# Kernel tuning notes

Hardware: AMD Instinct MI355X
Metric: run time of the kernel (lower is better)

The kernel has to match this reference:

```python
import jax, jax.numpy as jnp
import numpy as np

B, N, T_OBS, T_S, D, D_H, P = 32, 256, 50, 25, 128, 256, 8
TWO_PI = 2.0 * np.pi
EPS = 1e-4


def setup_inputs() -> dict:
    key = jax.random.key(0)
    ks = jax.random.split(key, 12)
    s = 0.02
    return {
        "x_ego_mean": jax.random.normal(ks[0], (B, T_OBS, 2), jnp.float32),
        "x_nei_mean": jax.random.normal(ks[1], (B, N, T_OBS, 2), jnp.float32),
        "f_ego": jax.random.normal(ks[2], (B, T_S, D), jnp.float32),
        "f_nei": jax.random.normal(ks[3], (B, N, T_S, D), jnp.float32),
        "W1": s * jax.random.normal(ks[4], (D, D_H), jnp.float32),
        "b1": jnp.zeros((D_H,), jnp.float32),
        "W2": s * jax.random.normal(ks[5], (D_H, D_H), jnp.float32),
        "b2": jnp.zeros((D_H,), jnp.float32),
        "W3": s * jax.random.normal(ks[6], (D_H, D // 2), jnp.float32),
        "b3": jnp.zeros((D // 2,), jnp.float32),
        "Wce": s * jax.random.normal(ks[7], (2, D // 2), jnp.float32),
        "bce": jnp.zeros((D // 2,), jnp.float32),
    }


def reference(x_ego_mean, x_nei_mean, f_ego, f_nei, W1, b1, W2, b2, W3, b3, Wce, bce):
    # --- spectral-similarity feature branch ---
    fn = f_ego[..., None, :, :] * f_nei            # [B, N, T_s, D]
    fn = jnp.max(fn, axis=-3)                      # max over neighbors -> [B, T_s, D]
    h = jax.nn.relu(fn @ W1 + b1)
    h = jax.nn.relu(h @ W2 + b2)
    fn = jax.nn.relu(h @ W3 + b3)                  # [B, T_s, D//2]

    # --- angle-based partitioning of relative positions ---
    t_r = int(np.ceil(x_ego_mean.shape[-2] / f_ego.shape[-2]))  # static stride
    p_nei = x_nei_mean - x_ego_mean[..., None, :, :]            # [B, N, T_obs, 2]
    p_nei = p_nei[..., ::t_r, :]                                # [B, N, T_s, 2]
    f_distance = jnp.linalg.norm(p_nei, axis=-1)                # [B, N, T_s]
    f_angle = jnp.mod(jnp.arctan2(p_nei[..., 0], p_nei[..., 1]), TWO_PI)
    pidx = (f_angle / (TWO_PI / P)).astype(jnp.int32)           # [B, N, T_s]

    nei_mask = (jnp.sum(jnp.abs(p_nei), axis=-1) != 0).astype(jnp.int32)
    non_self_mask = (f_distance > 0.005).astype(jnp.int32)
    final_mask = nei_mask * non_self_mask
    pidx = pidx * final_mask + (-1) * (1 - final_mask)          # invalid -> -1

    # one-hot over partitions replaces the per-partition python loop
    onehot = (pidx[..., None] == jnp.arange(P, dtype=jnp.int32)).astype(f_distance.dtype)  # [B,N,T_s,P]
    counts = jnp.sum(onehot, axis=-3)                           # [B, T_s, P]
    n = counts + EPS
    dist_mean = jnp.sum(f_distance[..., None] * onehot, axis=-3) / n   # [B, T_s, P]
    ang_mean = jnp.sum(f_angle[..., None] * onehot, axis=-3) / n       # [B, T_s, P]

    # original: y_p = sum_N(fn * mask)/n; fn has no N dim, so this is fn * counts / n
    y = fn[..., :, None, :] * (counts / n)[..., None]           # [B, T_s, P, D//2]

    positions = jnp.stack([dist_mean, ang_mean], axis=-1)       # [B, T_s, P, 2]
    pos_enc = jax.nn.relu(positions @ Wce + bce)                # [B, T_s, P, D//2]
    return jnp.concatenate([y, pos_enc], axis=-1)               # [B, T_s, P, D]
```

## Files before the change

### kernel.cpp

```cpp
#include <hip/hip_runtime.h>
#include <math.h>
#include <float.h>

#define B_ 32
#define N_ 256
#define T_OBS_ 50
#define T_S_ 25
#define D_ 128
#define D_H_ 256
#define P_ 8
#define PLANE_ (T_S_ * D_)
#define TG_ 13

static constexpr float TWO_PI_F = 6.2831854820251465f;
static constexpr float BIN_W_F = 0.78539818525314331f;
static constexpr float EPS_F = 1e-4f;

__global__ __launch_bounds__(512) void fused(
    const float* __restrict__ f_ego, const float* __restrict__ f_nei,
    const float* __restrict__ W1, const float* __restrict__ b1,
    const float* __restrict__ W2, const float* __restrict__ b2,
    const float* __restrict__ W3, const float* __restrict__ b3,
    const float* __restrict__ x_ego, const float* __restrict__ x_nei,
    const float* __restrict__ Wce, const float* __restrict__ bce,
    float* __restrict__ out) {
  __shared__ float spool[4096];
  __shared__ float sin_[2][D_];
  __shared__ float sh1[2][D_H_];
  __shared__ float sh2[2][D_H_];
  __shared__ float f3s[2][64];
  __shared__ float whc[8][P_], whd[8][P_], wha[8][P_];
  __shared__ float cnt[2][P_], dsum[2][P_], asum[2][P_];

  const int tid = threadIdx.x;
  const int b = blockIdx.x / TG_;
  const int g = blockIdx.x - b * TG_;
  const int t0 = 2 * g;
  const int t1 = (2 * g + 1 < T_S_) ? (2 * g + 1) : (T_S_ - 1);

  if (tid < 8 * P_) {
    (&whc[0][0])[tid] = 0.f;
    (&whd[0][0])[tid] = 0.f;
    (&wha[0][0])[tid] = 0.f;
  }

  {
    const int sub = tid & 63;
    const int lt = sub >> 5;
    const int d4 = sub & 31;
    const int ng = tid >> 6;
    const int t = lt ? t1 : t0;
    const float4 e =
        *(const float4*)(f_ego + ((size_t)b * T_S_ + t) * D_ + 4 * d4);
    const float* base = f_nei + (size_t)b * N_ * PLANE_ + t * D_ + 4 * d4;
    float4 m = make_float4(-FLT_MAX, -FLT_MAX, -FLT_MAX, -FLT_MAX);
#pragma unroll 16
    for (int i = 0; i < 32; ++i) {
      int n = ng + 8 * i;
      float4 v = *(const float4*)(base + (size_t)n * PLANE_);
      m.x = fmaxf(m.x, e.x * v.x);
      m.y = fmaxf(m.y, e.y * v.y);
      m.z = fmaxf(m.z, e.z * v.z);
      m.w = fmaxf(m.w, e.w * v.w);
    }
    ((float4*)spool)[ng * 64 + sub] = m;
  }

  float2 eg, xn;
  {
    int r = tid >> 8, n = tid & 255;
    int t = r ? t1 : t0;
    int tobs = 2 * t;
    eg = *(const float2*)&x_ego[((size_t)b * T_OBS_ + tobs) * 2];
    xn = *(const float2*)&x_nei[(((size_t)b * N_ + n) * T_OBS_ + tobs) * 2];
  }
  const float bb1 = b1[tid & 255];
  const float bb2 = b2[tid & 255];

  __syncthreads();

  if (tid < 64) {
    float4 r = ((float4*)spool)[tid];
#pragma unroll
    for (int ngg = 1; ngg < 8; ++ngg) {
      float4 v = ((float4*)spool)[ngg * 64 + tid];
      r.x = fmaxf(r.x, v.x);
      r.y = fmaxf(r.y, v.y);
      r.z = fmaxf(r.z, v.z);
      r.w = fmaxf(r.w, v.w);
    }
    *(float4*)&sin_[tid >> 5][4 * (tid & 31)] = r;
  }
  __syncthreads();

  {
    const int s = tid >> 6, j4 = tid & 63;
    const float4* W1v = (const float4*)W1;
    float a[2][4] = {};
#pragma unroll
    for (int kk = 0; kk < 16; ++kk) {
      int k = s * 16 + kk;
      float4 w = W1v[k * 64 + j4];
#pragma unroll
      for (int r = 0; r < 2; ++r) {
        float x = sin_[r][k];
        a[r][0] = fmaf(x, w.x, a[r][0]);
        a[r][1] = fmaf(x, w.y, a[r][1]);
        a[r][2] = fmaf(x, w.z, a[r][2]);
        a[r][3] = fmaf(x, w.w, a[r][3]);
      }
    }
#pragma unroll
    for (int r = 0; r < 2; ++r)
      *(float4*)&spool[(s * 2 + r) * 256 + 4 * j4] =
          make_float4(a[r][0], a[r][1], a[r][2], a[r][3]);
  }
  __syncthreads();
  {
    int r = tid >> 8, j = tid & 255;
    float sum = bb1;
#pragma unroll
    for (int s = 0; s < 8; ++s) sum += spool[(s * 2 + r) * 256 + j];
    sh1[r][j] = fmaxf(sum, 0.f);
  }
  __syncthreads();

  {
    const int s = tid >> 6, j4 = tid & 63;
    const float4* W2v = (const float4*)W2;
    float a[2][4] = {};
#pragma unroll
    for (int kk = 0; kk < 32; ++kk) {
      int k = s * 32 + kk;
      float4 w = W2v[k * 64 + j4];
#pragma unroll
      for (int r = 0; r < 2; ++r) {
        float x = sh1[r][k];
        a[r][0] = fmaf(x, w.x, a[r][0]);
        a[r][1] = fmaf(x, w.y, a[r][1]);
        a[r][2] = fmaf(x, w.z, a[r][2]);
        a[r][3] = fmaf(x, w.w, a[r][3]);
      }
    }
#pragma unroll
    for (int r = 0; r < 2; ++r)
      *(float4*)&spool[(s * 2 + r) * 256 + 4 * j4] =
          make_float4(a[r][0], a[r][1], a[r][2], a[r][3]);
  }
  __syncthreads();
  {
    int r = tid >> 8, j = tid & 255;
    float sum = bb2;
#pragma unroll
    for (int s = 0; s < 8; ++s) sum += spool[(s * 2 + r) * 256 + j];
    sh2[r][j] = fmaxf(sum, 0.f);
  }
  __syncthreads();

  {
    const int s3 = tid >> 4, j4 = tid & 15;
    const float4* W3v = (const float4*)W3;
    float a[2][4] = {};
#pragma unroll
    for (int kk = 0; kk < 8; ++kk) {
      int k = s3 * 8 + kk;
      float4 w = W3v[k * 16 + j4];
#pragma unroll
      for (int r = 0; r < 2; ++r) {
        float x = sh2[r][k];
        a[r][0] = fmaf(x, w.x, a[r][0]);
        a[r][1] = fmaf(x, w.y, a[r][1]);
        a[r][2] = fmaf(x, w.z, a[r][2]);
        a[r][3] = fmaf(x, w.w, a[r][3]);
      }
    }
#pragma unroll
    for (int r = 0; r < 2; ++r)
      *(float4*)&spool[(s3 * 2 + r) * 64 + 4 * j4] =
          make_float4(a[r][0], a[r][1], a[r][2], a[r][3]);
  }
  {
    const int w = tid >> 6;
    float p0 = xn.x - eg.x;
    float p1 = xn.y - eg.y;
    float dist = sqrtf(p0 * p0 + p1 * p1);
    float ang = atan2f(p0, p1);
    if (ang < 0.f) ang += TWO_PI_F;
    int pidx = (int)(ang / BIN_W_F);
    bool mask = ((fabsf(p0) + fabsf(p1)) != 0.f) && (dist > 0.005f);
    if (mask && pidx >= 0 && pidx < P_) {
      atomicAdd(&whc[w][pidx], 1.f);
      atomicAdd(&whd[w][pidx], dist);
      atomicAdd(&wha[w][pidx], ang);
    }
  }
  __syncthreads();

  if (tid < 2 * 64) {
    int r = tid >> 6, j = tid & 63;
    float sum = b3[j];
#pragma unroll
    for (int s = 0; s < 32; ++s) sum += spool[(s * 2 + r) * 64 + j];
    f3s[r][j] = fmaxf(sum, 0.f);
  }
  if (tid >= 128 && tid < 144) {
    int i = tid - 128;
    int r = i >> 3, p = i & 7;
    float c = 0.f, d = 0.f, a = 0.f;
#pragma unroll
    for (int w = 0; w < 4; ++w) {
      c += whc[r * 4 + w][p];
      d += whd[r * 4 + w][p];
      a += wha[r * 4 + w][p];
    }
    cnt[r][p] = c;
    dsum[r][p] = d;
    asum[r][p] = a;
  }
  __syncthreads();

  {
    int r = tid >> 8, i4 = tid & 255;
    int t = r ? t1 : t0;
    int p = i4 >> 5;
    int c0 = (i4 & 31) * 4;
    float nn = cnt[r][p] + EPS_F;
    float4 v;
    if (c0 < 64) {
      float sc = cnt[r][p] / nn;
      v = make_float4(f3s[r][c0 + 0] * sc, f3s[r][c0 + 1] * sc,
                      f3s[r][c0 + 2] * sc, f3s[r][c0 + 3] * sc);
    } else {
      int jj = c0 - 64;
      float dm = dsum[r][p] / nn;
      float am = asum[r][p] / nn;
      v.x = fmaxf(fmaf(dm, Wce[jj + 0], fmaf(am, Wce[64 + jj + 0], bce[jj + 0])), 0.f);
      v.y = fmaxf(fmaf(dm, Wce[jj + 1], fmaf(am, Wce[64 + jj + 1], bce[jj + 1])), 0.f);
      v.z = fmaxf(fmaf(dm, Wce[jj + 2], fmaf(am, Wce[64 + jj + 2], bce[jj + 2])), 0.f);
      v.w = fmaxf(fmaf(dm, Wce[jj + 3], fmaf(am, Wce[64 + jj + 3], bce[jj + 3])), 0.f);
    }
    *(float4*)(out + ((size_t)b * T_S_ + t) * 1024 + 4 * i4) = v;
  }
}

extern "C" void kernel_launch(void* const* d_in, const int* in_sizes, int n_in,
                              void* d_out, int out_size, void* d_ws,
                              size_t ws_size, hipStream_t stream) {
  const float* x_ego = (const float*)d_in[0];
  const float* x_nei = (const float*)d_in[1];
  const float* f_ego = (const float*)d_in[2];
  const float* f_nei = (const float*)d_in[3];
  const float* W1 = (const float*)d_in[4];
  const float* b1 = (const float*)d_in[5];
  const float* W2 = (const float*)d_in[6];
  const float* b2 = (const float*)d_in[7];
  const float* W3 = (const float*)d_in[8];
  const float* b3 = (const float*)d_in[9];
  const float* Wce = (const float*)d_in[10];
  const float* bce = (const float*)d_in[11];
  float* out = (float*)d_out;

  fused<<<B_ * TG_, 512, 0, stream>>>(f_ego, f_nei, W1, b1, W2, b2, W3, b3,
                                      x_ego, x_nei, Wce, bce, out);
}
```

Measured before the change: 34.26 us.

## Assign one time step per block instead of two to increase grid size

Changes the work split so each block handles a single (batch, time) pair, raising the grid from B*13 to B*25 blocks. The neighbor max-reduction now uses 16 neighbor groups over 32 d4 lanes, and the MLP stages process one row. This removes the duplicated last time step in odd tails and gives more blocks to fill the CUs. In exchange, each block reloads the full W1/W2/W3 weights for only one row, which doubles weight traffic per output row and lowers arithmetic reuse.

```diff
diff --git a/kernel.cpp b/kernel.cpp
--- a/kernel.cpp
+++ b/kernel.cpp
@@ -10,7 +10,6 @@
 #define D_H_ 256
 #define P_ 8
 #define PLANE_ (T_S_ * D_)
-#define TG_ 13
 
 static constexpr float TWO_PI_F = 6.2831854820251465f;
 static constexpr float BIN_W_F = 0.78539818525314331f;
@@ -24,162 +23,133 @@
     const float* __restrict__ x_ego, const float* __restrict__ x_nei,
     const float* __restrict__ Wce, const float* __restrict__ bce,
     float* __restrict__ out) {
-  __shared__ float spool[4096];
-  __shared__ float sin_[2][D_];
-  __shared__ float sh1[2][D_H_];
-  __shared__ float sh2[2][D_H_];
-  __shared__ float f3s[2][64];
-  __shared__ float whc[8][P_], whd[8][P_], wha[8][P_];
-  __shared__ float cnt[2][P_], dsum[2][P_], asum[2][P_];
+  __shared__ float spool[2048];
+  __shared__ float sin_[D_];
+  __shared__ float sh1[D_H_];
+  __shared__ float sh2[D_H_];
+  __shared__ float f3s[64];
+  __shared__ float whc[4][P_], whd[4][P_], wha[4][P_];
+  __shared__ float cnt[P_], dsum[P_], asum[P_];
 
   const int tid = threadIdx.x;
-  const int b = blockIdx.x / TG_;
-  const int g = blockIdx.x - b * TG_;
-  const int t0 = 2 * g;
-  const int t1 = (2 * g + 1 < T_S_) ? (2 * g + 1) : (T_S_ - 1);
-
-  if (tid < 8 * P_) {
+  const int b = blockIdx.x / T_S_;
+  const int t = blockIdx.x - b * T_S_;
+
+  if (tid < 4 * P_) {
     (&whc[0][0])[tid] = 0.f;
     (&whd[0][0])[tid] = 0.f;
     (&wha[0][0])[tid] = 0.f;
   }
 
   {
-    const int sub = tid & 63;
-    const int lt = sub >> 5;
-    const int d4 = sub & 31;
-    const int ng = tid >> 6;
-    const int t = lt ? t1 : t0;
+    const int ng = tid >> 5;
+    const int d4 = tid & 31;
     const float4 e =
         *(const float4*)(f_ego + ((size_t)b * T_S_ + t) * D_ + 4 * d4);
     const float* base = f_nei + (size_t)b * N_ * PLANE_ + t * D_ + 4 * d4;
     float4 m = make_float4(-FLT_MAX, -FLT_MAX, -FLT_MAX, -FLT_MAX);
 #pragma unroll 16
-    for (int i = 0; i < 32; ++i) {
-      int n = ng + 8 * i;
+    for (int i = 0; i < 16; ++i) {
+      int n = ng + 16 * i;
       float4 v = *(const float4*)(base + (size_t)n * PLANE_);
       m.x = fmaxf(m.x, e.x * v.x);
       m.y = fmaxf(m.y, e.y * v.y);
       m.z = fmaxf(m.z, e.z * v.z);
       m.w = fmaxf(m.w, e.w * v.w);
     }
-    ((float4*)spool)[ng * 64 + sub] = m;
+    ((float4*)spool)[ng * 32 + d4] = m;
   }
 
   float2 eg, xn;
-  {
-    int r = tid >> 8, n = tid & 255;
-    int t = r ? t1 : t0;
+  if (tid < 256) {
     int tobs = 2 * t;
     eg = *(const float2*)&x_ego[((size_t)b * T_OBS_ + tobs) * 2];
-    xn = *(const float2*)&x_nei[(((size_t)b * N_ + n) * T_OBS_ + tobs) * 2];
-  }
-  const float bb1 = b1[tid & 255];
-  const float bb2 = b2[tid & 255];
-
-  __syncthreads();
-
-  if (tid < 64) {
+    xn = *(const float2*)&x_nei[(((size_t)b * N_ + tid) * T_OBS_ + tobs) * 2];
+  }
+
+  __syncthreads();
+
+  if (tid < 32) {
     float4 r = ((float4*)spool)[tid];
 #pragma unroll
-    for (int ngg = 1; ngg < 8; ++ngg) {
-      float4 v = ((float4*)spool)[ngg * 64 + tid];
+    for (int ngg = 1; ngg < 16; ++ngg) {
+      float4 v = ((float4*)spool)[ngg * 32 + tid];
       r.x = fmaxf(r.x, v.x);
       r.y = fmaxf(r.y, v.y);
       r.z = fmaxf(r.z, v.z);
       r.w = fmaxf(r.w, v.w);
     }
-    *(float4*)&sin_[tid >> 5][4 * (tid & 31)] = r;
+    *(float4*)&sin_[4 * tid] = r;
   }
   __syncthreads();
 
   {
     const int s = tid >> 6, j4 = tid & 63;
     const float4* W1v = (const float4*)W1;
-    float a[2][4] = {};
+    float a0 = 0.f, a1 = 0.f, a2 = 0.f, a3 = 0.f;
 #pragma unroll
     for (int kk = 0; kk < 16; ++kk) {
       int k = s * 16 + kk;
       float4 w = W1v[k * 64 + j4];
-#pragma unroll
-      for (int r = 0; r < 2; ++r) {
-        float x = sin_[r][k];
-        a[r][0] = fmaf(x, w.x, a[r][0]);
-        a[r][1] = fmaf(x, w.y, a[r][1]);
-        a[r][2] = fmaf(x, w.z, a[r][2]);
-        a[r][3] = fmaf(x, w.w, a[r][3]);
-      }
-    }
-#pragma unroll
-    for (int r = 0; r < 2; ++r)
-      *(float4*)&spool[(s * 2 + r) * 256 + 4 * j4] =
-          make_float4(a[r][0], a[r][1], a[r][2], a[r][3]);
-  }
-  __syncthreads();
-  {
-    int r = tid >> 8, j = tid & 255;
-    float sum = bb1;
-#pragma unroll
-    for (int s = 0; s < 8; ++s) sum += spool[(s * 2 + r) * 256 + j];
-    sh1[r][j] = fmaxf(sum, 0.f);
+      float x = sin_[k];
+      a0 = fmaf(x, w.x, a0);
+      a1 = fmaf(x, w.y, a1);
+      a2 = fmaf(x, w.z, a2);
+      a3 = fmaf(x, w.w, a3);
+    }
+    *(float4*)&spool[s * 256 + 4 * j4] = make_float4(a0, a1, a2, a3);
+  }
+  __syncthreads();
+  if (tid < 256) {
+    float sum = b1[tid];
+#pragma unroll
+    for (int s = 0; s < 8; ++s) sum += spool[s * 256 + tid];
+    sh1[tid] = fmaxf(sum, 0.f);
   }
   __syncthreads();
 
   {
     const int s = tid >> 6, j4 = tid & 63;
     const float4* W2v = (const float4*)W2;
-    float a[2][4] = {};
+    float a0 = 0.f, a1 = 0.f, a2 = 0.f, a3 = 0.f;
 #pragma unroll
     for (int kk = 0; kk < 32; ++kk) {
       int k = s * 32 + kk;
       float4 w = W2v[k * 64 + j4];
-#pragma unroll
-      for (int r = 0; r < 2; ++r) {
-        float x = sh1[r][k];
-        a[r][0] = fmaf(x, w.x, a[r][0]);
-        a[r][1] = fmaf(x, w.y, a[r][1]);
-        a[r][2] = fmaf(x, w.z, a[r][2]);
-        a[r][3] = fmaf(x, w.w, a[r][3]);
-      }
-    }
-#pragma unroll
-    for (int r = 0; r < 2; ++r)
-      *(float4*)&spool[(s * 2 + r) * 256 + 4 * j4] =
-          make_float4(a[r][0], a[r][1], a[r][2], a[r][3]);
-  }
-  __syncthreads();
-  {
-    int r = tid >> 8, j = tid & 255;
-    float sum = bb2;
-#pragma unroll
-    for (int s = 0; s < 8; ++s) sum += spool[(s * 2 + r) * 256 + j];
-    sh2[r][j] = fmaxf(sum, 0.f);
+      float x = sh1[k];
+      a0 = fmaf(x, w.x, a0);
+      a1 = fmaf(x, w.y, a1);
+      a2 = fmaf(x, w.z, a2);
+      a3 = fmaf(x, w.w, a3);
+    }
+    *(float4*)&spool[s * 256 + 4 * j4] = make_float4(a0, a1, a2, a3);
+  }
+  __syncthreads();
+  if (tid < 256) {
+    float sum = b2[tid];
+#pragma unroll
+    for (int s = 0; s < 8; ++s) sum += spool[s * 256 + tid];
+    sh2[tid] = fmaxf(sum, 0.f);
   }
   __syncthreads();
 
   {
     const int s3 = tid >> 4, j4 = tid & 15;
     const float4* W3v = (const float4*)W3;
-    float a[2][4] = {};
+    float a0 = 0.f, a1 = 0.f, a2 = 0.f, a3 = 0.f;
 #pragma unroll
     for (int kk = 0; kk < 8; ++kk) {
       int k = s3 * 8 + kk;
       float4 w = W3v[k * 16 + j4];
-#pragma unroll
-      for (int r = 0; r < 2; ++r) {
-        float x = sh2[r][k];
-        a[r][0] = fmaf(x, w.x, a[r][0]);
-        a[r][1] = fmaf(x, w.y, a[r][1]);
-        a[r][2] = fmaf(x, w.z, a[r][2]);
-        a[r][3] = fmaf(x, w.w, a[r][3]);
-      }
-    }
-#pragma unroll
-    for (int r = 0; r < 2; ++r)
-      *(float4*)&spool[(s3 * 2 + r) * 64 + 4 * j4] =
-          make_float4(a[r][0], a[r][1], a[r][2], a[r][3]);
-  }
-  {
+      float x = sh2[k];
+      a0 = fmaf(x, w.x, a0);
+      a1 = fmaf(x, w.y, a1);
+      a2 = fmaf(x, w.z, a2);
+      a3 = fmaf(x, w.w, a3);
+    }
+    *(float4*)&spool[s3 * 64 + 4 * j4] = make_float4(a0, a1, a2, a3);
+  }
+  if (tid < 256) {
     const int w = tid >> 6;
     float p0 = xn.x - eg.x;
     float p1 = xn.y - eg.y;
@@ -196,50 +166,39 @@
   }
   __syncthreads();
 
-  if (tid < 2 * 64) {
-    int r = tid >> 6, j = tid & 63;
-    float sum = b3[j];
-#pragma unroll
-    for (int s = 0; s < 32; ++s) sum += spool[(s * 2 + r) * 64 + j];
-    f3s[r][j] = fmaxf(sum, 0.f);
-  }
-  if (tid >= 128 && tid < 144) {
-    int i = tid - 128;
-    int r = i >> 3, p = i & 7;
-    float c = 0.f, d = 0.f, a = 0.f;
-#pragma unroll
-    for (int w = 0; w < 4; ++w) {
-      c += whc[r * 4 + w][p];
-      d += whd[r * 4 + w][p];
-      a += wha[r * 4 + w][p];
-    }
-    cnt[r][p] = c;
-    dsum[r][p] = d;
-    asum[r][p] = a;
-  }
-  __syncthreads();
-
-  {
-    int r = tid >> 8, i4 = tid & 255;
-    int t = r ? t1 : t0;
-    int p = i4 >> 5;
-    int c0 = (i4 & 31) * 4;
-    float nn = cnt[r][p] + EPS_F;
+  if (tid < 64) {
+    float sum = b3[tid];
+#pragma unroll
+    for (int s = 0; s < 32; ++s) sum += spool[s * 64 + tid];
+    f3s[tid] = fmaxf(sum, 0.f);
+  }
+  if (tid >= 64 && tid < 72) {
+    int p = tid - 64;
+    cnt[p] = whc[0][p] + whc[1][p] + whc[2][p] + whc[3][p];
+    dsum[p] = whd[0][p] + whd[1][p] + whd[2][p] + whd[3][p];
+    asum[p] = wha[0][p] + wha[1][p] + wha[2][p] + wha[3][p];
+  }
+  __syncthreads();
+
+  if (tid < 256) {
+    int p = tid >> 5;
+    int c0 = (tid & 31) * 4;
+    float nn = cnt[p] + EPS_F;
     float4 v;
     if (c0 < 64) {
-      float sc = cnt[r][p] / nn;
-      v = make_float4(f3s[r][c0 + 0] * sc, f3s[r][c0 + 1] * sc,
-                      f3s[r][c0 + 2] * sc, f3s[r][c0 + 3] * sc);
+      float sc = cnt[p] / nn;
+      v = make_float4(f3s[c0 + 0] * sc, f3s[c0 + 1] * sc, f3s[c0 + 2] * sc,
+                      f3s[c0 + 3] * sc);
     } else {
       int jj = c0 - 64;
-      float dm = dsum[r][p] / nn;
-      float am = asum[r][p] / nn;
+      float dm = dsum[p] / nn;
+      float am = asum[p] / nn;
       v.x = fmaxf(fmaf(dm, Wce[jj + 0], fmaf(am, Wce[64 + jj + 0], bce[jj + 0])), 0.f);
       v.y = fmaxf(fmaf(dm, Wce[jj + 1], fmaf(am, Wce[64 + jj + 1], bce[jj + 1])), 0.f);
       v.z = fmaxf(fmaf(dm, Wce[jj + 2], fmaf(am, Wce[64 + jj + 2], bce[jj + 2])), 0.f);
       v.w = fmaxf(fmaf(dm, Wce[jj + 3], fmaf(am, Wce[64 + jj + 3], bce[jj + 3])), 0.f);
     }
-    *(float4*)(out + ((size_t)b * T_S_ + t) * 1024 + 4 * i4) = v;
+    *(float4*)(out + ((size_t)b * T_S_ + t) * 1024 + 4 * tid) = v;
   }
 }
 
@@ -260,6 +219,6 @@
   const float* bce = (const float*)d_in[11];
   float* out = (float*)d_out;
 
-  fused<<<B_ * TG_, 512, 0, stream>>>(f_ego, f_nei, W1, b1, W2, b2, W3, b3,
-                                      x_ego, x_nei, Wce, bce, out);
+  fused<<<B_ * T_S_, 512, 0, stream>>>(f_ego, f_nei, W1, b1, W2, b2, W3, b3,
+                                       x_ego, x_nei, Wce, bce, out);
 }
```

Measured after the change: 41.73 us. 1.22x slower.

## Process four timesteps per block to amortize MLP weight reads

Applied to the files above, without the earlier changes.

Each block now handles four timesteps instead of two, giving 224 blocks rather than 416. The three MLP weight matrices are read once per block and applied to four rows, so weight traffic per timestep is halved. Partition histograms now use shared atomics directly on the per-row counters instead of per-wave partial tables. The costs are fewer blocks to fill the GPU during the f_nei max-reduction, which is memory-bound, more redundant clamped work for the last group (timesteps 24-27 all map to 24), and double the LDS use per block.

```diff
diff --git a/kernel.cpp b/kernel.cpp
--- a/kernel.cpp
+++ b/kernel.cpp
@@ -10,7 +10,7 @@
 #define D_H_ 256
 #define P_ 8
 #define PLANE_ (T_S_ * D_)
-#define TG_ 13
+#define TQ_ 7
 
 static constexpr float TWO_PI_F = 6.2831854820251465f;
 static constexpr float BIN_W_F = 0.78539818525314331f;
@@ -24,222 +24,245 @@
     const float* __restrict__ x_ego, const float* __restrict__ x_nei,
     const float* __restrict__ Wce, const float* __restrict__ bce,
     float* __restrict__ out) {
-  __shared__ float spool[4096];
-  __shared__ float sin_[2][D_];
-  __shared__ float sh1[2][D_H_];
-  __shared__ float sh2[2][D_H_];
-  __shared__ float f3s[2][64];
-  __shared__ float whc[8][P_], whd[8][P_], wha[8][P_];
-  __shared__ float cnt[2][P_], dsum[2][P_], asum[2][P_];
+  __shared__ float spool[8192];
+  __shared__ float sinv[4][D_];
+  __shared__ float sh1[4][D_H_];
+  __shared__ float sh2[4][D_H_];
+  __shared__ float f3s[4][64];
+  __shared__ float cnt[4][P_], dsum[4][P_], asum[4][P_];
 
   const int tid = threadIdx.x;
-  const int b = blockIdx.x / TG_;
-  const int g = blockIdx.x - b * TG_;
-  const int t0 = 2 * g;
-  const int t1 = (2 * g + 1 < T_S_) ? (2 * g + 1) : (T_S_ - 1);
-
-  if (tid < 8 * P_) {
-    (&whc[0][0])[tid] = 0.f;
-    (&whd[0][0])[tid] = 0.f;
-    (&wha[0][0])[tid] = 0.f;
-  }
-
-  {
-    const int sub = tid & 63;
+  const int b = blockIdx.x / TQ_;
+  const int q = blockIdx.x - b * TQ_;
+
+  if (tid < 96) {
+    (&cnt[0][0])[tid < 32 ? tid : tid] = 0.f;
+  }
+  if (tid < 32) (&cnt[0][0])[tid] = 0.f;
+  else if (tid < 64) (&dsum[0][0])[tid - 32] = 0.f;
+  else if (tid < 96) (&asum[0][0])[tid - 64] = 0.f;
+
+  {
+    const int sub = tid & 127;
+    const int ng = tid >> 7;
     const int lt = sub >> 5;
     const int d4 = sub & 31;
-    const int ng = tid >> 6;
-    const int t = lt ? t1 : t0;
+    int t = 4 * q + lt;
+    if (t > T_S_ - 1) t = T_S_ - 1;
     const float4 e =
         *(const float4*)(f_ego + ((size_t)b * T_S_ + t) * D_ + 4 * d4);
     const float* base = f_nei + (size_t)b * N_ * PLANE_ + t * D_ + 4 * d4;
     float4 m = make_float4(-FLT_MAX, -FLT_MAX, -FLT_MAX, -FLT_MAX);
 #pragma unroll 16
-    for (int i = 0; i < 32; ++i) {
-      int n = ng + 8 * i;
+    for (int i = 0; i < 64; ++i) {
+      int n = ng + 4 * i;
       float4 v = *(const float4*)(base + (size_t)n * PLANE_);
       m.x = fmaxf(m.x, e.x * v.x);
       m.y = fmaxf(m.y, e.y * v.y);
       m.z = fmaxf(m.z, e.z * v.z);
       m.w = fmaxf(m.w, e.w * v.w);
     }
-    ((float4*)spool)[ng * 64 + sub] = m;
-  }
-
-  float2 eg, xn;
-  {
-    int r = tid >> 8, n = tid & 255;
-    int t = r ? t1 : t0;
-    int tobs = 2 * t;
-    eg = *(const float2*)&x_ego[((size_t)b * T_OBS_ + tobs) * 2];
-    xn = *(const float2*)&x_nei[(((size_t)b * N_ + n) * T_OBS_ + tobs) * 2];
-  }
-  const float bb1 = b1[tid & 255];
-  const float bb2 = b2[tid & 255];
-
-  __syncthreads();
-
-  if (tid < 64) {
-    float4 r = ((float4*)spool)[tid];
-#pragma unroll
-    for (int ngg = 1; ngg < 8; ++ngg) {
-      float4 v = ((float4*)spool)[ngg * 64 + tid];
+    ((float4*)spool)[ng * 128 + sub] = m;
+  }
+
+  float2 eg0, xn0, eg1, xn1;
+  {
+    int r0 = tid >> 8, n0 = tid & 255;
+    int ta = 4 * q + r0;
+    if (ta > T_S_ - 1) ta = T_S_ - 1;
+    int tobs = 2 * ta;
+    eg0 = *(const float2*)&x_ego[((size_t)b * T_OBS_ + tobs) * 2];
+    xn0 = *(const float2*)&x_nei[(((size_t)b * N_ + n0) * T_OBS_ + tobs) * 2];
+    int i2 = tid + 512;
+    int r1 = i2 >> 8, n1 = i2 & 255;
+    int tb = 4 * q + r1;
+    if (tb > T_S_ - 1) tb = T_S_ - 1;
+    int tobs1 = 2 * tb;
+    eg1 = *(const float2*)&x_ego[((size_t)b * T_OBS_ + tobs1) * 2];
+    xn1 = *(const float2*)&x_nei[(((size_t)b * N_ + n1) * T_OBS_ + tobs1) * 2];
+  }
+  __syncthreads();
+
+  if (tid < 128) {
+    const float4* aPart = (const float4*)spool;
+    float4 r = aPart[tid];
+#pragma unroll
+    for (int g = 1; g < 4; ++g) {
+      float4 v = aPart[g * 128 + tid];
       r.x = fmaxf(r.x, v.x);
       r.y = fmaxf(r.y, v.y);
       r.z = fmaxf(r.z, v.z);
       r.w = fmaxf(r.w, v.w);
     }
-    *(float4*)&sin_[tid >> 5][4 * (tid & 31)] = r;
+    *(float4*)&sinv[tid >> 5][4 * (tid & 31)] = r;
   }
   __syncthreads();
 
   {
     const int s = tid >> 6, j4 = tid & 63;
-    const float4* W1v = (const float4*)W1;
-    float a[2][4] = {};
+    const float4* Wv = (const float4*)W1;
+    float a0[4], a1[4], a2[4], a3[4];
+#pragma unroll
+    for (int r = 0; r < 4; ++r) a0[r] = a1[r] = a2[r] = a3[r] = 0.f;
 #pragma unroll
     for (int kk = 0; kk < 16; ++kk) {
       int k = s * 16 + kk;
-      float4 w = W1v[k * 64 + j4];
-#pragma unroll
-      for (int r = 0; r < 2; ++r) {
-        float x = sin_[r][k];
-        a[r][0] = fmaf(x, w.x, a[r][0]);
-        a[r][1] = fmaf(x, w.y, a[r][1]);
-        a[r][2] = fmaf(x, w.z, a[r][2]);
-        a[r][3] = fmaf(x, w.w, a[r][3]);
-      }
-    }
-#pragma unroll
-    for (int r = 0; r < 2; ++r)
-      *(float4*)&spool[(s * 2 + r) * 256 + 4 * j4] =
-          make_float4(a[r][0], a[r][1], a[r][2], a[r][3]);
-  }
-  __syncthreads();
-  {
-    int r = tid >> 8, j = tid & 255;
-    float sum = bb1;
-#pragma unroll
-    for (int s = 0; s < 8; ++s) sum += spool[(s * 2 + r) * 256 + j];
-    sh1[r][j] = fmaxf(sum, 0.f);
+      float4 w = Wv[k * 64 + j4];
+#pragma unroll
+      for (int r = 0; r < 4; ++r) {
+        float x = sinv[r][k];
+        a0[r] = fmaf(x, w.x, a0[r]);
+        a1[r] = fmaf(x, w.y, a1[r]);
+        a2[r] = fmaf(x, w.z, a2[r]);
+        a3[r] = fmaf(x, w.w, a3[r]);
+      }
+    }
+#pragma unroll
+    for (int r = 0; r < 4; ++r)
+      *(float4*)&spool[(s * 4 + r) * 256 + 4 * j4] =
+          make_float4(a0[r], a1[r], a2[r], a3[r]);
+  }
+  __syncthreads();
+  {
+#pragma unroll
+    for (int rep = 0; rep < 2; ++rep) {
+      int idx = tid + rep * 512;
+      int r = idx >> 8, j = idx & 255;
+      float sum = b1[j];
+#pragma unroll
+      for (int s = 0; s < 8; ++s) sum += spool[(s * 4 + r) * 256 + j];
+      sh1[r][j] = fmaxf(sum, 0.f);
+    }
   }
   __syncthreads();
 
   {
     const int s = tid >> 6, j4 = tid & 63;
-    const float4* W2v = (const float4*)W2;
-    float a[2][4] = {};
+    const float4* Wv = (const float4*)W2;
+    float a0[4], a1[4], a2[4], a3[4];
+#pragma unroll
+    for (int r = 0; r < 4; ++r) a0[r] = a1[r] = a2[r] = a3[r] = 0.f;
 #pragma unroll
     for (int kk = 0; kk < 32; ++kk) {
       int k = s * 32 + kk;
-      float4 w = W2v[k * 64 + j4];
-#pragma unroll
-      for (int r = 0; r < 2; ++r) {
+      float4 w = Wv[k * 64 + j4];
+#pragma unroll
+      for (int r = 0; r < 4; ++r) {
         float x = sh1[r][k];
-        a[r][0] = fmaf(x, w.x, a[r][0]);
-        a[r][1] = fmaf(x, w.y, a[r][1]);
-        a[r][2] = fmaf(x, w.z, a[r][2]);
-        a[r][3] = fmaf(x, w.w, a[r][3]);
-      }
-    }
-#pragma unroll
-    for (int r = 0; r < 2; ++r)
-      *(float4*)&spool[(s * 2 + r) * 256 + 4 * j4] =
-          make_float4(a[r][0], a[r][1], a[r][2], a[r][3]);
-  }
-  __syncthreads();
-  {
-    int r = tid >> 8, j = tid & 255;
-    float sum = bb2;
-#pragma unroll
-    for (int s = 0; s < 8; ++s) sum += spool[(s * 2 + r) * 256 + j];
-    sh2[r][j] = fmaxf(sum, 0.f);
+        a0[r] = fmaf(x, w.x, a0[r]);
+        a1[r] = fmaf(x, w.y, a1[r]);
+        a2[r] = fmaf(x, w.z, a2[r]);
+        a3[r] = fmaf(x, w.w, a3[r]);
+      }
+    }
+#pragma unroll
+    for (int r = 0; r < 4; ++r)
+      *(float4*)&spool[(s * 4 + r) * 256 + 4 * j4] =
+          make_float4(a0[r], a1[r], a2[r], a3[r]);
+  }
+  __syncthreads();
+  {
+#pragma unroll
+    for (int rep = 0; rep < 2; ++rep) {
+      int idx = tid + rep * 512;
+      int r = idx >> 8, j = idx & 255;
+      float sum = b2[j];
+#pragma unroll
+      for (int s = 0; s < 8; ++s) sum += spool[(s * 4 + r) * 256 + j];
+      sh2[r][j] = fmaxf(sum, 0.f);
+    }
   }
   __syncthreads();
 
   {
     const int s3 = tid >> 4, j4 = tid & 15;
-    const float4* W3v = (const float4*)W3;
-    float a[2][4] = {};
+    const float4* Wv = (const float4*)W3;
+    float a0[4], a1[4], a2[4], a3[4];
+#pragma unroll
+    for (int r = 0; r < 4; ++r) a0[r] = a1[r] = a2[r] = a3[r] = 0.f;
 #pragma unroll
     for (int kk = 0; kk < 8; ++kk) {
       int k = s3 * 8 + kk;
-      float4 w = W3v[k * 16 + j4];
-#pragma unroll
-      for (int r = 0; r < 2; ++r) {
+      float4 w = Wv[k * 16 + j4];
+#pragma unroll
+      for (int r = 0; r < 4; ++r) {
         float x = sh2[r][k];
-        a[r][0] = fmaf(x, w.x, a[r][0]);
-        a[r][1] = fmaf(x, w.y, a[r][1]);
-        a[r][2] = fmaf(x, w.z, a[r][2]);
-        a[r][3] = fmaf(x, w.w, a[r][3]);
-      }
-    }
-#pragma unroll
-    for (int r = 0; r < 2; ++r)
-      *(float4*)&spool[(s3 * 2 + r) * 64 + 4 * j4] =
-          make_float4(a[r][0], a[r][1], a[r][2], a[r][3]);
-  }
-  {
-    const int w = tid >> 6;
-    float p0 = xn.x - eg.x;
-    float p1 = xn.y - eg.y;
+        a0[r] = fmaf(x, w.x, a0[r]);
+        a1[r] = fmaf(x, w.y, a1[r]);
+        a2[r] = fmaf(x, w.z, a2[r]);
+        a3[r] = fmaf(x, w.w, a3[r]);
+      }
+    }
+#pragma unroll
+    for (int r = 0; r < 4; ++r)
+      *(float4*)&spool[(s3 * 4 + r) * 64 + 4 * j4] =
+          make_float4(a0[r], a1[r], a2[r], a3[r]);
+  }
+  {
+    int r0 = tid >> 8;
+    float p0 = xn0.x - eg0.x;
+    float p1 = xn0.y - eg0.y;
     float dist = sqrtf(p0 * p0 + p1 * p1);
     float ang = atan2f(p0, p1);
     if (ang < 0.f) ang += TWO_PI_F;
     int pidx = (int)(ang / BIN_W_F);
     bool mask = ((fabsf(p0) + fabsf(p1)) != 0.f) && (dist > 0.005f);
     if (mask && pidx >= 0 && pidx < P_) {
-      atomicAdd(&whc[w][pidx], 1.f);
-      atomicAdd(&whd[w][pidx], dist);
-      atomicAdd(&wha[w][pidx], ang);
-    }
-  }
-  __syncthreads();
-
-  if (tid < 2 * 64) {
+      atomicAdd(&cnt[r0][pidx], 1.f);
+      atomicAdd(&dsum[r0][pidx], dist);
+      atomicAdd(&asum[r0][pidx], ang);
+    }
+    int r1 = (tid + 512) >> 8;
+    float q0 = xn1.x - eg1.x;
+    float q1 = xn1.y - eg1.y;
+    float dist2 = sqrtf(q0 * q0 + q1 * q1);
+    float ang2 = atan2f(q0, q1);
+    if (ang2 < 0.f) ang2 += TWO_PI_F;
+    int pidx2 = (int)(ang2 / BIN_W_F);
+    bool mask2 = ((fabsf(q0) + fabsf(q1)) != 0.f) && (dist2 > 0.005f);
+    if (mask2 && pidx2 >= 0 && pidx2 < P_) {
+      atomicAdd(&cnt[r1][pidx2], 1.f);
+      atomicAdd(&dsum[r1][pidx2], dist2);
+      atomicAdd(&asum[r1][pidx2], ang2);
+    }
+  }
+  __syncthreads();
+
+  if (tid < 256) {
     int r = tid >> 6, j = tid & 63;
     float sum = b3[j];
 #pragma unroll
-    for (int s = 0; s < 32; ++s) sum += spool[(s * 2 + r) * 64 + j];
+    for (int s = 0; s < 32; ++s) sum += spool[(s * 4 + r) * 64 + j];
     f3s[r][j] = fmaxf(sum, 0.f);
   }
-  if (tid >= 128 && tid < 144) {
-    int i = tid - 128;
-    int r = i >> 3, p = i & 7;
-    float c = 0.f, d = 0.f, a = 0.f;
-#pragma unroll
-    for (int w = 0; w < 4; ++w) {
-      c += whc[r * 4 + w][p];
-      d += whd[r * 4 + w][p];
-      a += wha[r * 4 + w][p];
-    }
-    cnt[r][p] = c;
-    dsum[r][p] = d;
-    asum[r][p] = a;
-  }
-  __syncthreads();
-
-  {
-    int r = tid >> 8, i4 = tid & 255;
-    int t = r ? t1 : t0;
-    int p = i4 >> 5;
-    int c0 = (i4 & 31) * 4;
-    float nn = cnt[r][p] + EPS_F;
-    float4 v;
-    if (c0 < 64) {
-      float sc = cnt[r][p] / nn;
-      v = make_float4(f3s[r][c0 + 0] * sc, f3s[r][c0 + 1] * sc,
-                      f3s[r][c0 + 2] * sc, f3s[r][c0 + 3] * sc);
-    } else {
-      int jj = c0 - 64;
-      float dm = dsum[r][p] / nn;
-      float am = asum[r][p] / nn;
-      v.x = fmaxf(fmaf(dm, Wce[jj + 0], fmaf(am, Wce[64 + jj + 0], bce[jj + 0])), 0.f);
-      v.y = fmaxf(fmaf(dm, Wce[jj + 1], fmaf(am, Wce[64 + jj + 1], bce[jj + 1])), 0.f);
-      v.z = fmaxf(fmaf(dm, Wce[jj + 2], fmaf(am, Wce[64 + jj + 2], bce[jj + 2])), 0.f);
-      v.w = fmaxf(fmaf(dm, Wce[jj + 3], fmaf(am, Wce[64 + jj + 3], bce[jj + 3])), 0.f);
-    }
-    *(float4*)(out + ((size_t)b * T_S_ + t) * 1024 + 4 * i4) = v;
+  __syncthreads();
+
+  {
+#pragma unroll
+    for (int rep = 0; rep < 2; ++rep) {
+      int idx = tid + rep * 512;
+      int r = idx >> 8, i4 = idx & 255;
+      int t = 4 * q + r;
+      if (t > T_S_ - 1) t = T_S_ - 1;
+      int p = i4 >> 5;
+      int c0 = (i4 & 31) * 4;
+      float nn = cnt[r][p] + EPS_F;
+      float4 v;
+      if (c0 < 64) {
+        float sc = cnt[r][p] / nn;
+        v = make_float4(f3s[r][c0 + 0] * sc, f3s[r][c0 + 1] * sc,
+                        f3s[r][c0 + 2] * sc, f3s[r][c0 + 3] * sc);
+      } else {
+        int jj = c0 - 64;
+        float dm = dsum[r][p] / nn;
+        float am = asum[r][p] / nn;
+        v.x = fmaxf(fmaf(dm, Wce[jj + 0], fmaf(am, Wce[64 + jj + 0], bce[jj + 0])), 0.f);
+        v.y = fmaxf(fmaf(dm, Wce[jj + 1], fmaf(am, Wce[64 + jj + 1], bce[jj + 1])), 0.f);
+        v.z = fmaxf(fmaf(dm, Wce[jj + 2], fmaf(am, Wce[64 + jj + 2], bce[jj + 2])), 0.f);
+        v.w = fmaxf(fmaf(dm, Wce[jj + 3], fmaf(am, Wce[64 + jj + 3], bce[jj + 3])), 0.f);
+      }
+      *(float4*)(out + ((size_t)b * T_S_ + t) * 1024 + 4 * i4) = v;
+    }
   }
 }
 
@@ -260,6 +283,6 @@
   const float* bce = (const float*)d_in[11];
   float* out = (float*)d_out;
 
-  fused<<<B_ * TG_, 512, 0, stream>>>(f_ego, f_nei, W1, b1, W2, b2, W3, b3,
+  fused<<<B_ * TQ_, 512, 0, stream>>>(f_ego, f_nei, W1, b1, W2, b2, W3, b3,
                                       x_ego, x_nei, Wce, bce, out);
 }
```

Measured after the change: 33.04 us. -3.6%, faster.
